# Performance work log

Measured on AMD Instinct MI355X. Metric: run time of the kernel, lower is better.

The kernel has to match this reference:

```python
import jax, jax.numpy as jnp
import numpy as np

N_HEADS = 16
N_EMBD = 1024

def setup_inputs() -> dict:
    key = jax.random.key(0)
    k1, k2, k3, k4, k5 = jax.random.split(key, 5)
    B, T, C = 4, 2048, N_EMBD
    x = jax.random.normal(k1, (B, T, C), dtype=jnp.float32)
    # Linear weights stored as [in, out] (equivalent math to torch's x @ W.T + b)
    W_attn = jax.random.normal(k2, (C, 3 * C), dtype=jnp.float32) * 0.02
    b_attn = jax.random.normal(k3, (3 * C,), dtype=jnp.float32) * 0.02
    W_proj = jax.random.normal(k4, (C, C), dtype=jnp.float32) * 0.02
    b_proj = jax.random.normal(k5, (C,), dtype=jnp.float32) * 0.02
    return {"x": x, "W_attn": W_attn, "b_attn": b_attn, "W_proj": W_proj, "b_proj": b_proj}

def reference(x, W_attn, b_attn, W_proj, b_proj):
    B, T, C = x.shape
    H = N_HEADS
    D = C // H
    scale = 1.0 / jnp.sqrt(jnp.asarray(D, dtype=x.dtype))
    # fused QKV projection
    qkv = x @ W_attn + b_attn                      # [B, T, 3C]
    q, k, v = jnp.split(qkv, 3, axis=-1)           # each [B, T, C]
    q = q.reshape(B, T, H, D)
    k = k.reshape(B, T, H, D)
    v = v.reshape(B, T, H, D)
    # non-causal SDPA
    scores = jnp.einsum('bqhd,bkhd->bhqk', q, k) * scale  # [B, H, T, T]
    attn = jax.nn.softmax(scores, axis=-1)
    y = jnp.einsum('bhqk,bkhd->bqhd', attn, v)     # [B, T, H, D]
    y = y.reshape(B, T, C)
    return y @ W_proj + b_proj
```

## Files before the change

kernel.cpp:

```cpp
#include <hip/hip_runtime.h>

typedef short s16x8 __attribute__((ext_vector_type(8)));
typedef short s16x4 __attribute__((ext_vector_type(4)));
typedef float f32x4 __attribute__((ext_vector_type(4)));

__device__ __forceinline__ unsigned short f2bf(float f) {
  unsigned u = __float_as_uint(f);
  u += 0x7fffu + ((u >> 16) & 1u);
  return (unsigned short)(u >> 16);
}
__device__ __forceinline__ float bf2f(unsigned short h) {
  return __uint_as_float(((unsigned)h) << 16);
}

#define GLOAD_LDS16(g, l)                                          \
  __builtin_amdgcn_global_load_lds(                                \
      (const __attribute__((address_space(1))) void*)(g),          \
      (__attribute__((address_space(3))) void*)(l), 16, 0, 0)


__global__ __launch_bounds__(256) void cvt_x_bf16(const float* __restrict__ in,
                                                  unsigned short* __restrict__ out) {
  int i = (blockIdx.x * 256 + threadIdx.x) * 4;
  float4 v = *(const float4*)(in + i);
  ushort4 o;
  o.x = f2bf(v.x); o.y = f2bf(v.y); o.z = f2bf(v.z); o.w = f2bf(v.w);
  *(ushort4*)(out + i) = o;
}

__global__ __launch_bounds__(256) void transpose_w(const float* __restrict__ W,
                                                   unsigned short* __restrict__ Wt,
                                                   int R, int C) {
  __shared__ float tile[32][33];
  int c0 = blockIdx.x * 32, r0 = blockIdx.y * 32;
  int x = threadIdx.x, ty = threadIdx.y;
  for (int yy = ty; yy < 32; yy += 8)
    tile[yy][x] = W[(size_t)(r0 + yy) * C + c0 + x];
  __syncthreads();
  for (int yy = ty; yy < 32; yy += 8)
    Wt[(size_t)(c0 + yy) * R + r0 + x] = f2bf(tile[x][yy]);
}

__global__ __launch_bounds__(256) void transpose_v(const unsigned short* __restrict__ qkv,
                                                   unsigned short* __restrict__ vt) {
  __shared__ unsigned short TT[32][72];
  const int bh = blockIdx.y;
  const int t0 = blockIdx.x * 32;
  const int b = bh >> 4, h = bh & 15;
  const int t = threadIdx.x;
  {
    int row = t >> 3, c8 = (t & 7) * 8;
    const unsigned short* src =
        qkv + (size_t)(b * 2048 + t0 + row) * 3072 + 2048 + h * 64 + c8;
    *(uint4*)&TT[row][c8] = *(const uint4*)src;
  }
  __syncthreads();
  {
    int drow = t >> 2, tc8 = (t & 3) * 8;
    uint4 val;
    unsigned short* vp = (unsigned short*)&val;
    for (int j = 0; j < 8; j++) vp[j] = TT[tc8 + j][drow];
    *(uint4*)(vt + (size_t)(bh * 64 + drow) * 2048 + t0 + tc8) = val;
  }
}


template <bool OUT_BF16>
__global__ __launch_bounds__(256) void gemm_bt(const unsigned short* __restrict__ A,
                                               const unsigned short* __restrict__ Bt,
                                               const float* __restrict__ bias,
                                               void* __restrict__ Cout,
                                               int M, int N, int K) {
  __shared__ __align__(16) unsigned short As[128 * 32];
  __shared__ __align__(16) unsigned short Bs[128 * 32];

  const int tid  = threadIdx.x;
  const int lane = tid & 63;
  const int w    = tid >> 6;
  const int lr   = lane & 15;
  const int quad = lane >> 4;
  const int wm   = (w >> 1) * 64;
  const int wn   = (w & 1) * 64;
  const int m0   = blockIdx.x * 128;
  const int n0   = blockIdx.y * 128;

  f32x4 acc[4][4];
  for (int i = 0; i < 4; i++)
    for (int j = 0; j < 4; j++)
      acc[i][j] = f32x4{0.f, 0.f, 0.f, 0.f};

  const int srow = tid >> 2;
  const int scb  = (tid & 3) * 8;
  const unsigned short* Ap = A  + (size_t)(m0 + srow) * K + scb;
  const unsigned short* Bp = Bt + (size_t)(n0 + srow) * K + scb;
  unsigned short* lA0 = As + w * 512;
  unsigned short* lA1 = As + 2048 + w * 512;
  unsigned short* lB0 = Bs + w * 512;
  unsigned short* lB1 = Bs + 2048 + w * 512;

  for (int kk = 0; kk < K; kk += 32) {
    __syncthreads();
    GLOAD_LDS16(Ap + kk, lA0);
    GLOAD_LDS16(Ap + (size_t)64 * K + kk, lA1);
    GLOAD_LDS16(Bp + kk, lB0);
    GLOAD_LDS16(Bp + (size_t)64 * K + kk, lB1);
    __syncthreads();

    s16x8 af[4], bf[4];
    for (int i = 0; i < 4; i++) af[i] = *(const s16x8*)&As[(wm + i * 16 + lr) * 32 + quad * 8];
    for (int j = 0; j < 4; j++) bf[j] = *(const s16x8*)&Bs[(wn + j * 16 + lr) * 32 + quad * 8];
    for (int i = 0; i < 4; i++)
      for (int j = 0; j < 4; j++)
        acc[i][j] = __builtin_amdgcn_mfma_f32_16x16x32_bf16(af[i], bf[j], acc[i][j], 0, 0, 0);
  }

  for (int j = 0; j < 4; j++) {
    int col = n0 + wn + j * 16 + lr;
    float bc = bias[col];
    for (int i = 0; i < 4; i++) {
      int rowb = m0 + wm + i * 16 + quad * 4;
      for (int r = 0; r < 4; r++) {
        float v = acc[i][j][r] + bc;
        if (OUT_BF16)
          ((unsigned short*)Cout)[(size_t)(rowb + r) * N + col] = f2bf(v);
        else
          ((float*)Cout)[(size_t)(rowb + r) * N + col] = v;
      }
    }
  }
}


__global__ __launch_bounds__(256, 4) void attn_flash(const unsigned short* __restrict__ qkv,
                                                     const unsigned short* __restrict__ vt,
                                                     unsigned short* __restrict__ y) {
  const int T = 2048, C3 = 3072;
  const int bh = blockIdx.x & 63;
  const int qt = blockIdx.x >> 6;
  const int b  = bh >> 4;
  const int h  = bh & 15;
  const int q0 = qt * 128;

  const int tid  = threadIdx.x;
  const int lane = tid & 63;
  const int w    = tid >> 6;
  const int lr   = lane & 15;
  const int quad = lane >> 4;

  __shared__ __align__(16) unsigned short Ks[2][64][64];
  __shared__ __align__(16) unsigned short Vs[2][64][64];

  s16x8 qf[2][2];
  const float QSC = 0.18033688f;
  for (int j = 0; j < 2; j++)
    for (int c = 0; c < 2; c++) {
      const unsigned short* qp =
          qkv + (size_t)(b * T + q0 + w * 32 + j * 16 + lr) * C3 + h * 64 + c * 32 + quad * 8;
      s16x8 t = *(const s16x8*)qp;
      s16x8 o;
      for (int e = 0; e < 8; e++)
        o[e] = (short)f2bf(bf2f((unsigned short)t[e]) * QSC);
      qf[j][c] = o;
    }

  s16x8 ones;
  for (int e = 0; e < 8; e++) ones[e] = (short)0x3F80;

  f32x4 O[2][4];
  f32x4 Lacc[2];
  for (int j = 0; j < 2; j++) {
    for (int dt = 0; dt < 4; dt++) O[j][dt] = f32x4{0.f, 0.f, 0.f, 0.f};
    Lacc[j] = f32x4{0.f, 0.f, 0.f, 0.f};
  }

  const int srow = tid >> 3;
  const int scol = (((tid & 7) ^ (srow & 7)) * 8);
  const int kperm = (((srow & 12) << 1) | ((srow >> 4) << 2) | (srow & 3));

  const unsigned short* kbase = qkv + (size_t)(b * T) * C3 + 1024 + (size_t)h * 64;
  const unsigned short* vbase = vt + (size_t)(bh * 64) * 2048;
  const unsigned short* kp0 = kbase + (size_t)(kperm)      * C3 + scol;
  const unsigned short* kp1 = kbase + (size_t)(32 + kperm) * C3 + scol;
  const unsigned short* vp0 = vbase + (size_t)(srow)      * 2048 + scol;
  const unsigned short* vp1 = vbase + (size_t)(srow + 32) * 2048 + scol;

#define STAGE_KV(bb, k0off)                                                  \
  do {                                                                       \
    GLOAD_LDS16(kp0 + (size_t)(k0off) * C3, &Ks[bb][w * 8][0]);              \
    GLOAD_LDS16(kp1 + (size_t)(k0off) * C3, &Ks[bb][w * 8 + 32][0]);         \
    GLOAD_LDS16(vp0 + (k0off), &Vs[bb][w * 8][0]);                           \
    GLOAD_LDS16(vp1 + (k0off), &Vs[bb][w * 8 + 32][0]);                      \
  } while (0)

  const int rswz = (lr & 7) << 4;

  STAGE_KV(0, 0);
  int cur = 0;
  for (int kt = 0; kt < 32; kt++) {
    __syncthreads();
    if (kt < 31) STAGE_KV(cur ^ 1, (kt + 1) * 64);

    const char* KsB = (const char*)&Ks[cur][0][0];
    const char* VsB = (const char*)&Vs[cur][0][0];

    for (int ch = 0; ch < 2; ch++) {
      const char* krowA = KsB + (ch * 32 + lr) * 128;
      const char* krowB = KsB + (ch * 32 + 16 + lr) * 128;
      s16x8 kA0 = *(const s16x8*)(krowA + ((quad * 16) ^ rswz));
      s16x8 kA1 = *(const s16x8*)(krowA + ((64 + quad * 16) ^ rswz));
      s16x8 kB0 = *(const s16x8*)(krowB + ((quad * 16) ^ rswz));
      s16x8 kB1 = *(const s16x8*)(krowB + ((64 + quad * 16) ^ rswz));
      s16x8 vf[4];
      for (int dt = 0; dt < 4; dt++)
        vf[dt] = *(const s16x8*)(VsB + (dt * 16 + lr) * 128 + ((ch * 64 + quad * 16) ^ rswz));

      for (int j = 0; j < 2; j++) {
        f32x4 Sa = f32x4{0.f, 0.f, 0.f, 0.f};
        f32x4 Sb = f32x4{0.f, 0.f, 0.f, 0.f};
        Sa = __builtin_amdgcn_mfma_f32_16x16x32_bf16(kA0, qf[j][0], Sa, 0, 0, 0);
        Sa = __builtin_amdgcn_mfma_f32_16x16x32_bf16(kA1, qf[j][1], Sa, 0, 0, 0);
        Sb = __builtin_amdgcn_mfma_f32_16x16x32_bf16(kB0, qf[j][0], Sb, 0, 0, 0);
        Sb = __builtin_amdgcn_mfma_f32_16x16x32_bf16(kB1, qf[j][1], Sb, 0, 0, 0);
        unsigned u0 = __float_as_uint(__builtin_amdgcn_exp2f(Sa[0])) + 0x8000u;
        unsigned u1 = __float_as_uint(__builtin_amdgcn_exp2f(Sa[1])) + 0x8000u;
        unsigned u2 = __float_as_uint(__builtin_amdgcn_exp2f(Sa[2])) + 0x8000u;
        unsigned u3 = __float_as_uint(__builtin_amdgcn_exp2f(Sa[3])) + 0x8000u;
        unsigned u4 = __float_as_uint(__builtin_amdgcn_exp2f(Sb[0])) + 0x8000u;
        unsigned u5 = __float_as_uint(__builtin_amdgcn_exp2f(Sb[1])) + 0x8000u;
        unsigned u6 = __float_as_uint(__builtin_amdgcn_exp2f(Sb[2])) + 0x8000u;
        unsigned u7 = __float_as_uint(__builtin_amdgcn_exp2f(Sb[3])) + 0x8000u;
        union { unsigned u[4]; s16x8 v; } pk;
        pk.u[0] = __builtin_amdgcn_perm(u1, u0, 0x07060302u);
        pk.u[1] = __builtin_amdgcn_perm(u3, u2, 0x07060302u);
        pk.u[2] = __builtin_amdgcn_perm(u5, u4, 0x07060302u);
        pk.u[3] = __builtin_amdgcn_perm(u7, u6, 0x07060302u);
        Lacc[j] = __builtin_amdgcn_mfma_f32_16x16x32_bf16(pk.v, ones, Lacc[j], 0, 0, 0);
        for (int dt = 0; dt < 4; dt++)
          O[j][dt] = __builtin_amdgcn_mfma_f32_16x16x32_bf16(pk.v, vf[dt], O[j][dt], 0, 0, 0);
      }
    }
    cur ^= 1;
  }
#undef STAGE_KV

  for (int j = 0; j < 2; j++) {
    for (int r = 0; r < 4; r++) {
      float inv = 1.f / Lacc[j][r];
      int row = b * T + q0 + w * 32 + j * 16 + quad * 4 + r;
      for (int dt = 0; dt < 4; dt++) {
        int col = h * 64 + dt * 16 + lr;
        y[(size_t)row * 1024 + col] = f2bf(O[j][dt][r] * inv);
      }
    }
  }
}


extern "C" void kernel_launch(void* const* d_in, const int* in_sizes, int n_in,
                              void* d_out, int out_size, void* d_ws, size_t ws_size,
                              hipStream_t stream) {
  const float* x  = (const float*)d_in[0];
  const float* Wa = (const float*)d_in[1];
  const float* ba = (const float*)d_in[2];
  const float* Wp = (const float*)d_in[3];
  const float* bp = (const float*)d_in[4];
  float* out = (float*)d_out;

  char* ws = (char*)d_ws;
  unsigned short* xb  = (unsigned short*)ws;
  unsigned short* Wat = (unsigned short*)(ws + 16777216);
  unsigned short* Wpt = (unsigned short*)(ws + 23068672);
  unsigned short* qkv = (unsigned short*)(ws + 25165824);
  unsigned short* vtr = (unsigned short*)(ws + 75497472);

  cvt_x_bf16<<<8192, 256, 0, stream>>>(x, xb);
  transpose_w<<<dim3(96, 32), dim3(32, 8), 0, stream>>>(Wa, Wat, 1024, 3072);
  transpose_w<<<dim3(32, 32), dim3(32, 8), 0, stream>>>(Wp, Wpt, 1024, 1024);

  gemm_bt<true><<<dim3(64, 24), 256, 0, stream>>>(xb, Wat, ba, qkv, 8192, 3072, 1024);

  transpose_v<<<dim3(64, 64), 256, 0, stream>>>(qkv, vtr);

  attn_flash<<<1024, 256, 0, stream>>>(qkv, vtr, xb);

  gemm_bt<false><<<dim3(64, 8), 256, 0, stream>>>(xb, Wpt, bp, out, 8192, 1024, 1024);
}
```

Baseline: 280.1 us.

## Double-buffer GEMM LDS tiles, switch to 32x32x16 MFMA with XOR swizzle

Rewrites the bf16 GEMM main loop to double-buffer the LDS tiles, issuing the global-to-LDS loads for the next K-slice before computing the current one, so there is one barrier per iteration instead of two. It also moves from 16x16x32 to 32x32x16 MFMA instructions with a 2x2 per-wave tile, which reduces the number of LDS fragment reads per MFMA. It adds an XOR swizzle on the LDS column placement to avoid bank conflicts. LDS use doubles, and the single barrier relies on the async global_load_lds being complete when the next barrier is reached, which is a correctness risk if the compiler does not insert the proper vmcnt waits.

```diff
diff --git a/kernel.cpp b/kernel.cpp
--- a/kernel.cpp
+++ b/kernel.cpp
@@ -3,6 +3,7 @@
 typedef short s16x8 __attribute__((ext_vector_type(8)));
 typedef short s16x4 __attribute__((ext_vector_type(4)));
 typedef float f32x4 __attribute__((ext_vector_type(4)));
+typedef float f32x16 __attribute__((ext_vector_type(16)));
 
 __device__ __forceinline__ unsigned short f2bf(float f) {
   unsigned u = __float_as_uint(f);
@@ -71,60 +72,77 @@
                                                const float* __restrict__ bias,
                                                void* __restrict__ Cout,
                                                int M, int N, int K) {
-  __shared__ __align__(16) unsigned short As[128 * 32];
-  __shared__ __align__(16) unsigned short Bs[128 * 32];
+  __shared__ __align__(16) unsigned short As[2][128 * 32];
+  __shared__ __align__(16) unsigned short Bs[2][128 * 32];
 
   const int tid  = threadIdx.x;
   const int lane = tid & 63;
   const int w    = tid >> 6;
-  const int lr   = lane & 15;
-  const int quad = lane >> 4;
+  const int lm   = lane & 31;
+  const int l5   = lane >> 5;
   const int wm   = (w >> 1) * 64;
   const int wn   = (w & 1) * 64;
   const int m0   = blockIdx.x * 128;
   const int n0   = blockIdx.y * 128;
 
-  f32x4 acc[4][4];
-  for (int i = 0; i < 4; i++)
-    for (int j = 0; j < 4; j++)
-      acc[i][j] = f32x4{0.f, 0.f, 0.f, 0.f};
+  f32x16 acc[2][2];
+  for (int i = 0; i < 2; i++)
+    for (int j = 0; j < 2; j++)
+      for (int r = 0; r < 16; r++) acc[i][j][r] = 0.f;
 
   const int srow = tid >> 2;
-  const int scb  = (tid & 3) * 8;
+  const int scb  = (((tid & 3) ^ (srow & 3)) * 8);
   const unsigned short* Ap = A  + (size_t)(m0 + srow) * K + scb;
   const unsigned short* Bp = Bt + (size_t)(n0 + srow) * K + scb;
-  unsigned short* lA0 = As + w * 512;
-  unsigned short* lA1 = As + 2048 + w * 512;
-  unsigned short* lB0 = Bs + w * 512;
-  unsigned short* lB1 = Bs + 2048 + w * 512;
-
+
+#define STAGE_G(bb, kk)                                                  \
+  do {                                                                   \
+    GLOAD_LDS16(Ap + (kk), &As[bb][w * 512]);                            \
+    GLOAD_LDS16(Ap + (size_t)64 * K + (kk), &As[bb][2048 + w * 512]);    \
+    GLOAD_LDS16(Bp + (kk), &Bs[bb][w * 512]);                            \
+    GLOAD_LDS16(Bp + (size_t)64 * K + (kk), &Bs[bb][2048 + w * 512]);    \
+  } while (0)
+
+  const int rx = (lm & 3) << 4;
+
+  STAGE_G(0, 0);
+  int cur = 0;
   for (int kk = 0; kk < K; kk += 32) {
     __syncthreads();
-    GLOAD_LDS16(Ap + kk, lA0);
-    GLOAD_LDS16(Ap + (size_t)64 * K + kk, lA1);
-    GLOAD_LDS16(Bp + kk, lB0);
-    GLOAD_LDS16(Bp + (size_t)64 * K + kk, lB1);
-    __syncthreads();
-
-    s16x8 af[4], bf[4];
-    for (int i = 0; i < 4; i++) af[i] = *(const s16x8*)&As[(wm + i * 16 + lr) * 32 + quad * 8];
-    for (int j = 0; j < 4; j++) bf[j] = *(const s16x8*)&Bs[(wn + j * 16 + lr) * 32 + quad * 8];
-    for (int i = 0; i < 4; i++)
-      for (int j = 0; j < 4; j++)
-        acc[i][j] = __builtin_amdgcn_mfma_f32_16x16x32_bf16(af[i], bf[j], acc[i][j], 0, 0, 0);
-  }
-
-  for (int j = 0; j < 4; j++) {
-    int col = n0 + wn + j * 16 + lr;
+    if (kk + 32 < K) STAGE_G(cur ^ 1, kk + 32);
+
+    const char* Ab = (const char*)As[cur];
+    const char* Bb = (const char*)Bs[cur];
+    s16x8 af[2][2], bfr[2][2];
+    for (int i = 0; i < 2; i++)
+      for (int ks = 0; ks < 2; ks++)
+        af[i][ks] = *(const s16x8*)(Ab + (wm + i * 32 + lm) * 64 +
+                                    (((l5 * 16 + ks * 32)) ^ rx));
+    for (int j = 0; j < 2; j++)
+      for (int ks = 0; ks < 2; ks++)
+        bfr[j][ks] = *(const s16x8*)(Bb + (wn + j * 32 + lm) * 64 +
+                                     (((l5 * 16 + ks * 32)) ^ rx));
+    for (int ks = 0; ks < 2; ks++)
+      for (int i = 0; i < 2; i++)
+        for (int j = 0; j < 2; j++)
+          acc[i][j] = __builtin_amdgcn_mfma_f32_32x32x16_bf16(af[i][ks], bfr[j][ks],
+                                                              acc[i][j], 0, 0, 0);
+    cur ^= 1;
+  }
+#undef STAGE_G
+
+  for (int j = 0; j < 2; j++) {
+    int col = n0 + wn + j * 32 + lm;
     float bc = bias[col];
-    for (int i = 0; i < 4; i++) {
-      int rowb = m0 + wm + i * 16 + quad * 4;
-      for (int r = 0; r < 4; r++) {
+    for (int i = 0; i < 2; i++) {
+      int rowb = m0 + wm + i * 32 + l5 * 4;
+      for (int r = 0; r < 16; r++) {
+        int row = rowb + (r & 3) + 8 * (r >> 2);
         float v = acc[i][j][r] + bc;
         if (OUT_BF16)
-          ((unsigned short*)Cout)[(size_t)(rowb + r) * N + col] = f2bf(v);
+          ((unsigned short*)Cout)[(size_t)row * N + col] = f2bf(v);
         else
-          ((float*)Cout)[(size_t)(rowb + r) * N + col] = v;
+          ((float*)Cout)[(size_t)row * N + col] = v;
       }
     }
   }
```

New measurement: 281.9 us. About the same (+0.6%).
